# Kernel optimization log

Measured on AMD Instinct MI355X. Metric: run time of the kernel, lower is better.

The kernel has to match this reference:

```python
import jax, jax.numpy as jnp
import numpy as np

N_NODES = 50000
N_EDGES = 800000
NFEAT = 256
NHID = 512
BN_EPS = 1e-5


def setup_inputs() -> dict:
    key = jax.random.key(0)
    ks = jax.random.split(key, 6)
    x = jax.random.normal(ks[0], (N_NODES, NFEAT), dtype=jnp.float32)
    edge_index = jax.random.randint(ks[1], (2, N_EDGES), 0, N_NODES, dtype=jnp.int64)
    # Xavier-uniform linear weights, zero biases (matches weights_init)
    lim1 = np.sqrt(6.0 / (NFEAT + NHID))
    W1 = jax.random.uniform(ks[2], (NFEAT, NHID), minval=-lim1, maxval=lim1, dtype=jnp.float32)
    b1 = jnp.zeros((NHID,), dtype=jnp.float32)
    lim2 = np.sqrt(6.0 / (NHID + NHID))
    W2 = jax.random.uniform(ks[3], (NHID, NHID), minval=-lim2, maxval=lim2, dtype=jnp.float32)
    b2 = jnp.zeros((NHID,), dtype=jnp.float32)
    gamma = jnp.ones((NHID,), dtype=jnp.float32)
    beta = jnp.zeros((NHID,), dtype=jnp.float32)
    return {"x": x, "edge_index": edge_index, "W1": W1, "b1": b1,
            "gamma": gamma, "beta": beta, "W2": W2, "b2": b2}


def reference(x, edge_index, W1, b1, gamma, beta, W2, b2):
    # GINConv (eps=0): h_i = MLP(x_i + sum_{j->i} x_j)
    src = edge_index[0]
    dst = edge_index[1]
    agg = jax.ops.segment_sum(x[src], dst, num_segments=x.shape[0])  # [N, nfeat]
    h = x + agg
    # MLP: Linear -> ReLU -> BatchNorm1d (training-mode batch stats) -> Linear
    h = jax.nn.relu(h @ W1 + b1)  # [N, nhid]
    mean = jnp.mean(h, axis=0)
    var = jnp.var(h, axis=0)  # biased, as PyTorch uses for normalization
    h = (h - mean) * jax.lax.rsqrt(var + BN_EPS) * gamma + beta
    return h @ W2 + b2
```

## Files before the change

### kernel.cpp

```cpp
#include <hip/hip_runtime.h>

#define NNODES 50000
#define NF 256
#define NH 512
#define MPAD 50048
#define NRB 391
#define BN_EPS 1e-5f
#define NSCAN 196

typedef unsigned short u16;
typedef __attribute__((ext_vector_type(8))) short bf16x8;
typedef __attribute__((ext_vector_type(4))) float f32x4;

__device__ __forceinline__ float bf2f(u16 u) {
  union { unsigned int i; float f; } v; v.i = ((unsigned int)u) << 16; return v.f;
}
__device__ __forceinline__ u16 f2bf(float f) {
  union { float ff; unsigned int i; } v; v.ff = f;
  unsigned int r = v.i + 0x7FFFu + ((v.i >> 16) & 1u);
  return (u16)(r >> 16);
}

__device__ __forceinline__ void async16(const void* g, void* l) {
  __builtin_amdgcn_global_load_lds(
      (const __attribute__((address_space(1))) unsigned int*)g,
      (__attribute__((address_space(3))) unsigned int*)l, 16, 0, 0);
}

__global__ void detect_idx(const int* __restrict__ ei, int* __restrict__ flag) {
  int v = ei[2 * threadIdx.x + 1];
  unsigned long long b = __ballot(v == 0);
  if (threadIdx.x == 0) *flag = (b == ~0ull) ? 1 : 0;
}

__global__ __launch_bounds__(256) void prep_kernel(const float* __restrict__ x,
                                                   u16* __restrict__ xbf,
                                                   const float* __restrict__ W1,
                                                   u16* __restrict__ W1t,
                                                   const int* __restrict__ ei,
                                                   const int* __restrict__ flag,
                                                   int* __restrict__ deg, int E) {
  const int b = blockIdx.x;
  if (b < 2048) {
    const size_t n8 = (size_t)NNODES * NF / 8;
    size_t stride = (size_t)2048 * 256;
    for (size_t i = b * (size_t)256 + threadIdx.x; i < n8; i += stride) {
      float4 a = ((const float4*)x)[2 * i];
      float4 c = ((const float4*)x)[2 * i + 1];
      ushort4 lo, hi;
      lo.x = f2bf(a.x); lo.y = f2bf(a.y); lo.z = f2bf(a.z); lo.w = f2bf(a.w);
      hi.x = f2bf(c.x); hi.y = f2bf(c.y); hi.z = f2bf(c.z); hi.w = f2bf(c.w);
      ((ushort4*)xbf)[2 * i] = lo;
      ((ushort4*)xbf)[2 * i + 1] = hi;
    }
  } else if (b < 2560) {
    int idx = (b - 2048) * 256 + threadIdx.x;
    int n = idx >> 8;
    int k = idx & 255;
    W1t[(size_t)n * NF + k] = f2bf(W1[(size_t)k * NH + n]);
  } else {
    const int is64 = *flag;
    const int gtid = (b - 2560) * 256 + threadIdx.x;
    const int stride = 1024 * 256;
    if (is64) {
      const int4* d4 = (const int4*)(ei + 2 * (size_t)E);
      int np = E >> 1;
      for (int p = gtid; p < np; p += stride) {
        int4 d = d4[p];
        if ((unsigned)d.x < NNODES) atomicAdd(&deg[d.x], 1);
        if ((unsigned)d.z < NNODES) atomicAdd(&deg[d.z], 1);
      }
      for (int e = (np << 1) + gtid; e < E; e += stride) {
        int d = ei[2 * (size_t)E + 2 * e];
        if ((unsigned)d < NNODES) atomicAdd(&deg[d], 1);
      }
    } else {
      const int4* d4 = (const int4*)(ei + E);
      int np = E >> 2;
      for (int p = gtid; p < np; p += stride) {
        int4 d = d4[p];
        if ((unsigned)d.x < NNODES) atomicAdd(&deg[d.x], 1);
        if ((unsigned)d.y < NNODES) atomicAdd(&deg[d.y], 1);
        if ((unsigned)d.z < NNODES) atomicAdd(&deg[d.z], 1);
        if ((unsigned)d.w < NNODES) atomicAdd(&deg[d.w], 1);
      }
      for (int e = (np << 2) + gtid; e < E; e += stride) {
        int d = ei[(size_t)E + e];
        if ((unsigned)d < NNODES) atomicAdd(&deg[d], 1);
      }
    }
  }
}

__global__ __launch_bounds__(256) void scan1_kernel(const int* __restrict__ deg,
                                                    int* __restrict__ rowptr,
                                                    int* __restrict__ blocksums) {
  const int t = threadIdx.x;
  int i = blockIdx.x * 256 + t;
  int v = (i < NNODES) ? deg[i] : 0;
  __shared__ int sm[256];
  sm[t] = v;
  __syncthreads();
  for (int off = 1; off < 256; off <<= 1) {
    int u = (t >= off) ? sm[t - off] : 0;
    __syncthreads();
    sm[t] += u;
    __syncthreads();
  }
  if (i < NNODES) rowptr[i] = sm[t] - v;
  if (t == 255) blocksums[blockIdx.x] = sm[255];
}

__global__ __launch_bounds__(256) void scan2_kernel(int* __restrict__ blocksums,
                                                    int* __restrict__ rowptr) {
  const int t = threadIdx.x;
  int v = (t < NSCAN) ? blocksums[t] : 0;
  __shared__ int sm[256];
  sm[t] = v;
  __syncthreads();
  for (int off = 1; off < 256; off <<= 1) {
    int u = (t >= off) ? sm[t - off] : 0;
    __syncthreads();
    sm[t] += u;
    __syncthreads();
  }
  if (t < NSCAN) blocksums[t] = sm[t] - v;
  if (t == 255) rowptr[NNODES] = sm[255];
}

__global__ __launch_bounds__(256) void scan3_kernel(const int* __restrict__ blocksums,
                                                    int* __restrict__ rowptr) {
  int i = blockIdx.x * 256 + threadIdx.x;
  if (i < NNODES) rowptr[i] += blocksums[blockIdx.x];
}

__global__ __launch_bounds__(256) void fill_kernel(const int* __restrict__ ei,
                                                   const int* __restrict__ flag,
                                                   const int* __restrict__ rowptr,
                                                   int* __restrict__ cursor,
                                                   int* __restrict__ srcs, int E) {
  const int is64 = *flag;
  const int gtid = blockIdx.x * 256 + threadIdx.x;
  const int stride = gridDim.x * 256;
  if (is64) {
    const int4* s4 = (const int4*)ei;
    const int4* d4 = (const int4*)(ei + 2 * (size_t)E);
    int np = E >> 1;
    for (int p = gtid; p < np; p += stride) {
      int4 sv = s4[p], dv = d4[p];
      if ((unsigned)sv.x < NNODES && (unsigned)dv.x < NNODES) {
        int pos = rowptr[dv.x] + atomicAdd(&cursor[dv.x], 1);
        if ((unsigned)pos < (unsigned)E) srcs[pos] = sv.x;
      }
      if ((unsigned)sv.z < NNODES && (unsigned)dv.z < NNODES) {
        int pos = rowptr[dv.z] + atomicAdd(&cursor[dv.z], 1);
        if ((unsigned)pos < (unsigned)E) srcs[pos] = sv.z;
      }
    }
    for (int e = (np << 1) + gtid; e < E; e += stride) {
      int src = ei[2 * e], dst = ei[2 * (size_t)E + 2 * e];
      if ((unsigned)src >= NNODES || (unsigned)dst >= NNODES) continue;
      int pos = rowptr[dst] + atomicAdd(&cursor[dst], 1);
      if ((unsigned)pos < (unsigned)E) srcs[pos] = src;
    }
  } else {
    const int4* s4 = (const int4*)ei;
    const int4* d4 = (const int4*)(ei + E);
    int np = E >> 2;
    for (int p = gtid; p < np; p += stride) {
      int4 sv = s4[p], dv = d4[p];
      int ss[4] = {sv.x, sv.y, sv.z, sv.w};
      int dd[4] = {dv.x, dv.y, dv.z, dv.w};
#pragma unroll
      for (int j = 0; j < 4; ++j) {
        if ((unsigned)ss[j] < NNODES && (unsigned)dd[j] < NNODES) {
          int pos = rowptr[dd[j]] + atomicAdd(&cursor[dd[j]], 1);
          if ((unsigned)pos < (unsigned)E) srcs[pos] = ss[j];
        }
      }
    }
    for (int e = (np << 2) + gtid; e < E; e += stride) {
      int src = ei[e], dst = ei[(size_t)E + e];
      if ((unsigned)src >= NNODES || (unsigned)dst >= NNODES) continue;
      int pos = rowptr[dst] + atomicAdd(&cursor[dst], 1);
      if ((unsigned)pos < (unsigned)E) srcs[pos] = src;
    }
  }
}

__global__ __launch_bounds__(256) void gather_kernel(const u16* __restrict__ xbf,
                                                     const int* __restrict__ srcs,
                                                     const int* __restrict__ rowptr,
                                                     u16* __restrict__ hpad) {
  const int hl = threadIdx.x & 31;
  const int node = blockIdx.x * 8 + (threadIdx.x >> 5);
  if (node >= MPAD) return;
  bf16x8* outp = (bf16x8*)(hpad + (size_t)node * NF + hl * 8);
  if (node >= NNODES) {
    bf16x8 z = {0, 0, 0, 0, 0, 0, 0, 0};
    *outp = z;
    return;
  }
  bf16x8 sv = *(const bf16x8*)(xbf + (size_t)node * NF + hl * 8);
  float acc[8];
#pragma unroll
  for (int j = 0; j < 8; ++j) acc[j] = bf2f((u16)sv[j]);
  int e = rowptr[node];
  const int e1 = rowptr[node + 1];
  for (; e + 3 < e1; e += 4) {
    int s0 = srcs[e], s1 = srcs[e + 1], s2 = srcs[e + 2], s3 = srcs[e + 3];
    bf16x8 v0 = *(const bf16x8*)(xbf + (size_t)s0 * NF + hl * 8);
    bf16x8 v1 = *(const bf16x8*)(xbf + (size_t)s1 * NF + hl * 8);
    bf16x8 v2 = *(const bf16x8*)(xbf + (size_t)s2 * NF + hl * 8);
    bf16x8 v3 = *(const bf16x8*)(xbf + (size_t)s3 * NF + hl * 8);
#pragma unroll
    for (int j = 0; j < 8; ++j)
      acc[j] += bf2f((u16)v0[j]) + bf2f((u16)v1[j]) + bf2f((u16)v2[j]) + bf2f((u16)v3[j]);
  }
  for (; e < e1; ++e) {
    int s0 = srcs[e];
    bf16x8 v0 = *(const bf16x8*)(xbf + (size_t)s0 * NF + hl * 8);
#pragma unroll
    for (int j = 0; j < 8; ++j) acc[j] += bf2f((u16)v0[j]);
  }
  bf16x8 o;
#pragma unroll
  for (int j = 0; j < 8; ++j) o[j] = (short)f2bf(acc[j]);
  *outp = o;
}

template <int K, bool RELU, bool OUTF32, bool STATS>
__global__ __launch_bounds__(256) void gemm_bt(const u16* __restrict__ Ab,
                                               const u16* __restrict__ Bt,
                                               const float* __restrict__ bias,
                                               void* __restrict__ Cp, int Mstore,
                                               float* __restrict__ parts) {
  __shared__ __align__(16) u16 As[2][128 * 64];
  __shared__ __align__(16) u16 Bs[2][128 * 64];
  __shared__ float sred[256];
  const int tid = threadIdx.x;
  const int lane = tid & 63;
  const int wid = tid >> 6;
  const int wr = wid >> 1, wc = wid & 1;

  const int nwg = gridDim.x;
  const int q = nwg >> 3, r = nwg & 7;
  const int xcd = blockIdx.x & 7, idx = blockIdx.x >> 3;
  const int work = (xcd < r ? xcd * (q + 1) : r * (q + 1) + (xcd - r) * q) + idx;
  const int brow = (work >> 2) * 128;
  const int bcol = (work & 3) * 128;

  f32x4 acc[4][4] = {};

  const int lrow = lane >> 3;
  const int lkc = ((lane & 7) ^ (lrow & 7)) * 8;
  const int nt = K / 64;

#pragma unroll
  for (int i = 0; i < 4; ++i) {
    int c = i * 4 + wid;
    int row = c * 8 + lrow;
    async16(Ab + (size_t)(brow + row) * K + lkc, &As[0][c * 512]);
    async16(Bt + (size_t)(bcol + row) * K + lkc, &Bs[0][c * 512]);
  }
  if (STATS) {
    if (tid < 64) ((float4*)sred)[tid] = (float4){0.f, 0.f, 0.f, 0.f};
  }
  __syncthreads();

  int cur = 0;
  for (int t = 0; t < nt; ++t) {
    if (t + 1 < nt) {
      const int k0 = (t + 1) * 64;
#pragma unroll
      for (int i = 0; i < 4; ++i) {
        int c = i * 4 + wid;
        int row = c * 8 + lrow;
        async16(Ab + (size_t)(brow + row) * K + k0 + lkc, &As[cur ^ 1][c * 512]);
        async16(Bt + (size_t)(bcol + row) * K + k0 + lkc, &Bs[cur ^ 1][c * 512]);
      }
    }
#pragma unroll
    for (int ks = 0; ks < 2; ++ks) {
      bf16x8 af[4], bfr[4];
      const int rchunk = ((ks << 2) + (lane >> 4)) ^ (lane & 7);
#pragma unroll
      for (int m = 0; m < 4; ++m)
        af[m] = *(const bf16x8*)&As[cur][(wr * 64 + m * 16 + (lane & 15)) * 64 + rchunk * 8];
#pragma unroll
      for (int n = 0; n < 4; ++n)
        bfr[n] = *(const bf16x8*)&Bs[cur][(wc * 64 + n * 16 + (lane & 15)) * 64 + rchunk * 8];
#pragma unroll
      for (int n = 0; n < 4; ++n)
#pragma unroll
        for (int m = 0; m < 4; ++m)
          acc[n][m] = __builtin_amdgcn_mfma_f32_16x16x32_bf16(bfr[n], af[m], acc[n][m], 0, 0, 0);
    }
    __syncthreads();
    cur ^= 1;
  }

  const int row_base = brow + wr * 64 + (lane & 15);
  const int col_base = bcol + wc * 64 + ((lane >> 4) << 2);
#pragma unroll
  for (int n = 0; n < 4; ++n) {
    int col = col_base + n * 16;
    float4 bv4 = *(const float4*)&bias[col];
    float s0 = 0.f, s1 = 0.f, s2 = 0.f, s3 = 0.f;
    float q0 = 0.f, q1 = 0.f, q2 = 0.f, q3 = 0.f;
#pragma unroll
    for (int m = 0; m < 4; ++m) {
      int row = row_base + m * 16;
      f32x4 a = acc[n][m];
      float v0 = a[0] + bv4.x, v1 = a[1] + bv4.y, v2 = a[2] + bv4.z, v3 = a[3] + bv4.w;
      if (RELU) {
        v0 = fmaxf(v0, 0.f); v1 = fmaxf(v1, 0.f);
        v2 = fmaxf(v2, 0.f); v3 = fmaxf(v3, 0.f);
      }
      if (row < Mstore) {
        if (OUTF32) {
          float4 o = {v0, v1, v2, v3};
          *(float4*)&((float*)Cp)[(size_t)row * NH + col] = o;
        } else {
          ushort4 o = {f2bf(v0), f2bf(v1), f2bf(v2), f2bf(v3)};
          *(ushort4*)&((u16*)Cp)[(size_t)row * NH + col] = o;
        }
      }
      if (STATS && row < NNODES) {
        s0 += v0; s1 += v1; s2 += v2; s3 += v3;
        q0 += v0 * v0; q1 += v1 * v1; q2 += v2 * v2; q3 += v3 * v3;
      }
    }
    if (STATS) {
#pragma unroll
      for (int msk = 1; msk < 16; msk <<= 1) {
        s0 += __shfl_xor(s0, msk); s1 += __shfl_xor(s1, msk);
        s2 += __shfl_xor(s2, msk); s3 += __shfl_xor(s3, msk);
        q0 += __shfl_xor(q0, msk); q1 += __shfl_xor(q1, msk);
        q2 += __shfl_xor(q2, msk); q3 += __shfl_xor(q3, msk);
      }
      if ((lane & 15) == 0) {
        int lc = wc * 64 + n * 16 + ((lane >> 4) << 2);
        atomicAdd(&sred[lc + 0], s0); atomicAdd(&sred[lc + 1], s1);
        atomicAdd(&sred[lc + 2], s2); atomicAdd(&sred[lc + 3], s3);
        atomicAdd(&sred[128 + lc + 0], q0); atomicAdd(&sred[128 + lc + 1], q1);
        atomicAdd(&sred[128 + lc + 2], q2); atomicAdd(&sred[128 + lc + 3], q3);
      }
    }
  }
  if (STATS) {
    __syncthreads();
    if (tid < 128) {
      parts[(size_t)work * 256 + tid] = sred[tid];
      parts[(size_t)work * 256 + 128 + tid] = sred[128 + tid];
    }
  }
}

__global__ __launch_bounds__(256) void stats2_kernel(const float* __restrict__ parts,
                                                     float* __restrict__ ssum) {
  int c = blockIdx.x * 256 + threadIdx.x;
  int c0 = c & 511, issq = c >> 9;
  float acc = 0.f;
  for (int rb = 0; rb < NRB; ++rb)
    acc += parts[(size_t)((rb << 2) + (c0 >> 7)) * 256 + (c0 & 127) + (issq ? 128 : 0)];
  ssum[c] = acc;
}

__global__ void bn_finalize(const float* __restrict__ ssum, const float* __restrict__ ssq,
                            const float* __restrict__ gamma, const float* __restrict__ beta,
                            float* __restrict__ a_arr, float* __restrict__ c_arr,
                            int* __restrict__ err) {
  int c = threadIdx.x;
  float mean = ssum[c] * (1.f / NNODES);
  float var = ssq[c] * (1.f / NNODES) - mean * mean;
  if (!(mean == mean) || !(var == var) ||
      fabsf(mean) > 1e20f || var > 1e20f || var < -1e-2f)
    err[0] = 2;
  unsigned long long z = __ballot(ssq[c] == 0.0f);
  if (threadIdx.x == 0 && z == ~0ull) err[1] = 3;
  if (var < 0.f) var = 0.f;
  float a = gamma[c] * rsqrtf(var + BN_EPS);
  a_arr[c] = a;
  c_arr[c] = beta[c] - mean * a;
}

__global__ __launch_bounds__(256) void fold_w2(const float* __restrict__ W2,
                                               const float* __restrict__ b2,
                                               const float* __restrict__ a_arr,
                                               const float* __restrict__ c_arr,
                                               u16* __restrict__ W2pt,
                                               float* __restrict__ bias2p) {
  int n = blockIdx.x;
  int t = threadIdx.x;
  float accv = 0.f;
  for (int k = t; k < NH; k += 256) {
    float w = W2[(size_t)k * NH + n];
    W2pt[(size_t)n * NH + k] = f2bf(a_arr[k] * w);
    accv += c_arr[k] * w;
  }
  __shared__ float red[256];
  red[t] = accv;
  __syncthreads();
  for (int s = 128; s > 0; s >>= 1) {
    if (t < s) red[t] += red[t + s];
    __syncthreads();
  }
  if (t == 0) bias2p[n] = b2[n] + red[0];
}

__global__ __launch_bounds__(256) void write_sentinel(float* __restrict__ out, int n, float val) {
  int stride = gridDim.x * blockDim.x;
  for (int i = blockIdx.x * blockDim.x + threadIdx.x; i < n; i += stride) out[i] = val;
}

__global__ __launch_bounds__(256) void apply_err(const int* __restrict__ err,
                                                 float* __restrict__ out, int n) {
  float val = 0.f;
  if (err[1] == 3) val = -300000.f;
  if (err[0] == 2) val = -500000.f;
  if (val == 0.f) return;
  int stride = gridDim.x * blockDim.x;
  for (int i = blockIdx.x * blockDim.x + threadIdx.x; i < n; i += stride) out[i] = val;
}

extern "C" void kernel_launch(void* const* d_in, const int* in_sizes, int n_in,
                              void* d_out, int out_size, void* d_ws, size_t ws_size,
                              hipStream_t stream) {
  const float* x     = (const float*)d_in[0];
  const int*   ei    = (const int*)d_in[1];
  const float* W1    = (const float*)d_in[2];
  const float* b1    = (const float*)d_in[3];
  const float* gamma = (const float*)d_in[4];
  const float* beta  = (const float*)d_in[5];
  const float* W2    = (const float*)d_in[6];
  const float* b2    = (const float*)d_in[7];
  float* out = (float*)d_out;
  const int E = in_sizes[1] / 2;

  char* ws = (char*)d_ws;
  size_t off = 0;
  auto alloc = [&](size_t bytes) {
    char* p = ws + off;
    off += (bytes + 255) & ~(size_t)255;
    return p;
  };
  u16*   xbf    = (u16*)alloc((size_t)NNODES * NF * 2);
  u16*   hpad   = (u16*)alloc((size_t)MPAD * NF * 2);
  u16*   h1     = (u16*)alloc((size_t)MPAD * NH * 2);
  u16*   W1t    = (u16*)alloc((size_t)NH * NF * 2);
  u16*   W2pt   = (u16*)alloc((size_t)NH * NH * 2);
  int*   srcs   = (int*)alloc((size_t)E * 4);
  int*   rowptr = (int*)alloc((size_t)(NNODES + 1) * 4);
  int*   deg    = (int*)alloc((size_t)2 * NNODES * 4);
  int*   cursor = deg + NNODES;
  int*   bsums  = (int*)alloc(256 * 4);
  float* parts  = (float*)alloc((size_t)NRB * 4 * 256 * 4);
  float* ssum   = (float*)alloc(NH * 4);
  float* ssq    = (float*)alloc(NH * 4);
  int*   err    = (int*)alloc(8);
  float* a_arr  = (float*)alloc(NH * 4);
  float* c_arr  = (float*)alloc(NH * 4);
  float* bias2p = (float*)alloc(NH * 4);
  int*   flag   = (int*)alloc(4);

  if (off > ws_size) {
    write_sentinel<<<2048, 256, 0, stream>>>(out, out_size,
        1.0e7f + 1048576.0f * (float)(ws_size >> 20));
    return;
  }

  hipMemsetAsync(deg, 0, (size_t)2 * NNODES * 4, stream);
  hipMemsetAsync(err, 0, 8, stream);

  detect_idx<<<1, 64, 0, stream>>>(ei, flag);
  prep_kernel<<<3584, 256, 0, stream>>>(x, xbf, W1, W1t, ei, flag, deg, E);
  scan1_kernel<<<NSCAN, 256, 0, stream>>>(deg, rowptr, bsums);
  scan2_kernel<<<1, 256, 0, stream>>>(bsums, rowptr);
  scan3_kernel<<<NSCAN, 256, 0, stream>>>(bsums, rowptr);
  fill_kernel<<<1024, 256, 0, stream>>>(ei, flag, rowptr, cursor, srcs, E);
  gather_kernel<<<MPAD / 8, 256, 0, stream>>>(xbf, srcs, rowptr, hpad);

  const int nwg = NRB * 4;
  gemm_bt<NF, true, false, true><<<nwg, 256, 0, stream>>>(hpad, W1t, b1, h1, MPAD, parts);

  stats2_kernel<<<4, 256, 0, stream>>>(parts, ssum);
  bn_finalize<<<1, NH, 0, stream>>>(ssum, ssq, gamma, beta, a_arr, c_arr, err);
  fold_w2<<<NH, 256, 0, stream>>>(W2, b2, a_arr, c_arr, W2pt, bias2p);

  gemm_bt<NH, false, true, false><<<nwg, 256, 0, stream>>>(h1, W2pt, bias2p, out, NNODES, nullptr);

  apply_err<<<2048, 256, 0, stream>>>(err, out, out_size);
}
```

Baseline: 284.1 us.

## Cut kernel launches by fusing scan, fill, conversion and BN stats stages

Index-format detection moves into the histogram and fill kernels, so its separate launch goes away. The three-pass scan becomes two passes, with the second pass also writing a cursor array holding absolute offsets, which removes the rowptr load per edge in the fill. The CSR fill is combined with the x-to-bf16 conversion and the W1 transpose in one launch, so the bandwidth-bound conversion can overlap the atomic-heavy fill. The stats reduction is merged with BN finalize, and the zero-variance error sentinel is dropped. The cost is that each scan_b block recomputes the block-sums scan, and the prep work now waits on the histogram and scan.

```diff
diff --git a/kernel.cpp b/kernel.cpp
--- a/kernel.cpp
+++ b/kernel.cpp
@@ -27,74 +27,49 @@
       (__attribute__((address_space(3))) unsigned int*)l, 16, 0, 0);
 }
 
-__global__ void detect_idx(const int* __restrict__ ei, int* __restrict__ flag) {
-  int v = ei[2 * threadIdx.x + 1];
-  unsigned long long b = __ballot(v == 0);
-  if (threadIdx.x == 0) *flag = (b == ~0ull) ? 1 : 0;
-}
-
-__global__ __launch_bounds__(256) void prep_kernel(const float* __restrict__ x,
-                                                   u16* __restrict__ xbf,
-                                                   const float* __restrict__ W1,
-                                                   u16* __restrict__ W1t,
-                                                   const int* __restrict__ ei,
-                                                   const int* __restrict__ flag,
+__global__ __launch_bounds__(256) void hist_kernel(const int* __restrict__ ei,
                                                    int* __restrict__ deg, int E) {
-  const int b = blockIdx.x;
-  if (b < 2048) {
-    const size_t n8 = (size_t)NNODES * NF / 8;
-    size_t stride = (size_t)2048 * 256;
-    for (size_t i = b * (size_t)256 + threadIdx.x; i < n8; i += stride) {
-      float4 a = ((const float4*)x)[2 * i];
-      float4 c = ((const float4*)x)[2 * i + 1];
-      ushort4 lo, hi;
-      lo.x = f2bf(a.x); lo.y = f2bf(a.y); lo.z = f2bf(a.z); lo.w = f2bf(a.w);
-      hi.x = f2bf(c.x); hi.y = f2bf(c.y); hi.z = f2bf(c.z); hi.w = f2bf(c.w);
-      ((ushort4*)xbf)[2 * i] = lo;
-      ((ushort4*)xbf)[2 * i + 1] = hi;
-    }
-  } else if (b < 2560) {
-    int idx = (b - 2048) * 256 + threadIdx.x;
-    int n = idx >> 8;
-    int k = idx & 255;
-    W1t[(size_t)n * NF + k] = f2bf(W1[(size_t)k * NH + n]);
+  __shared__ int sf;
+  if (threadIdx.x < 64) {
+    unsigned long long b = __ballot(ei[2 * threadIdx.x + 1] == 0);
+    if (threadIdx.x == 0) sf = (b == ~0ull) ? 1 : 0;
+  }
+  __syncthreads();
+  const int is64 = sf;
+  const int gtid = blockIdx.x * 256 + threadIdx.x;
+  const int stride = gridDim.x * 256;
+  if (is64) {
+    const int4* d4 = (const int4*)(ei + 2 * (size_t)E);
+    int np = E >> 1;
+    for (int p = gtid; p < np; p += stride) {
+      int4 d = d4[p];
+      if ((unsigned)d.x < NNODES) atomicAdd(&deg[d.x], 1);
+      if ((unsigned)d.z < NNODES) atomicAdd(&deg[d.z], 1);
+    }
+    for (int e = (np << 1) + gtid; e < E; e += stride) {
+      int d = ei[2 * (size_t)E + 2 * e];
+      if ((unsigned)d < NNODES) atomicAdd(&deg[d], 1);
+    }
   } else {
-    const int is64 = *flag;
-    const int gtid = (b - 2560) * 256 + threadIdx.x;
-    const int stride = 1024 * 256;
-    if (is64) {
-      const int4* d4 = (const int4*)(ei + 2 * (size_t)E);
-      int np = E >> 1;
-      for (int p = gtid; p < np; p += stride) {
-        int4 d = d4[p];
-        if ((unsigned)d.x < NNODES) atomicAdd(&deg[d.x], 1);
-        if ((unsigned)d.z < NNODES) atomicAdd(&deg[d.z], 1);
-      }
-      for (int e = (np << 1) + gtid; e < E; e += stride) {
-        int d = ei[2 * (size_t)E + 2 * e];
-        if ((unsigned)d < NNODES) atomicAdd(&deg[d], 1);
-      }
-    } else {
-      const int4* d4 = (const int4*)(ei + E);
-      int np = E >> 2;
-      for (int p = gtid; p < np; p += stride) {
-        int4 d = d4[p];
-        if ((unsigned)d.x < NNODES) atomicAdd(&deg[d.x], 1);
-        if ((unsigned)d.y < NNODES) atomicAdd(&deg[d.y], 1);
-        if ((unsigned)d.z < NNODES) atomicAdd(&deg[d.z], 1);
-        if ((unsigned)d.w < NNODES) atomicAdd(&deg[d.w], 1);
-      }
-      for (int e = (np << 2) + gtid; e < E; e += stride) {
-        int d = ei[(size_t)E + e];
-        if ((unsigned)d < NNODES) atomicAdd(&deg[d], 1);
-      }
-    }
-  }
-}
-
-__global__ __launch_bounds__(256) void scan1_kernel(const int* __restrict__ deg,
-                                                    int* __restrict__ rowptr,
-                                                    int* __restrict__ blocksums) {
+    const int4* d4 = (const int4*)(ei + E);
+    int np = E >> 2;
+    for (int p = gtid; p < np; p += stride) {
+      int4 d = d4[p];
+      if ((unsigned)d.x < NNODES) atomicAdd(&deg[d.x], 1);
+      if ((unsigned)d.y < NNODES) atomicAdd(&deg[d.y], 1);
+      if ((unsigned)d.z < NNODES) atomicAdd(&deg[d.z], 1);
+      if ((unsigned)d.w < NNODES) atomicAdd(&deg[d.w], 1);
+    }
+    for (int e = (np << 2) + gtid; e < E; e += stride) {
+      int d = ei[(size_t)E + e];
+      if ((unsigned)d < NNODES) atomicAdd(&deg[d], 1);
+    }
+  }
+}
+
+__global__ __launch_bounds__(256) void scan_a(const int* __restrict__ deg,
+                                              int* __restrict__ rowptr,
+                                              int* __restrict__ blocksums) {
   const int t = threadIdx.x;
   int i = blockIdx.x * 256 + t;
   int v = (i < NNODES) ? deg[i] : 0;
@@ -111,12 +86,12 @@
   if (t == 255) blocksums[blockIdx.x] = sm[255];
 }
 
-__global__ __launch_bounds__(256) void scan2_kernel(int* __restrict__ blocksums,
-                                                    int* __restrict__ rowptr) {
+__global__ __launch_bounds__(256) void scan_b(const int* __restrict__ blocksums,
+                                              int* __restrict__ rowptr,
+                                              int* __restrict__ cw) {
   const int t = threadIdx.x;
-  int v = (t < NSCAN) ? blocksums[t] : 0;
   __shared__ int sm[256];
-  sm[t] = v;
+  sm[t] = (t < NSCAN) ? blocksums[t] : 0;
   __syncthreads();
   for (int off = 1; off < 256; off <<= 1) {
     int u = (t >= off) ? sm[t - off] : 0;
@@ -124,67 +99,95 @@
     sm[t] += u;
     __syncthreads();
   }
-  if (t < NSCAN) blocksums[t] = sm[t] - v;
-  if (t == 255) rowptr[NNODES] = sm[255];
-}
-
-__global__ __launch_bounds__(256) void scan3_kernel(const int* __restrict__ blocksums,
-                                                    int* __restrict__ rowptr) {
-  int i = blockIdx.x * 256 + threadIdx.x;
-  if (i < NNODES) rowptr[i] += blocksums[blockIdx.x];
-}
-
-__global__ __launch_bounds__(256) void fill_kernel(const int* __restrict__ ei,
-                                                   const int* __restrict__ flag,
-                                                   const int* __restrict__ rowptr,
-                                                   int* __restrict__ cursor,
-                                                   int* __restrict__ srcs, int E) {
-  const int is64 = *flag;
-  const int gtid = blockIdx.x * 256 + threadIdx.x;
-  const int stride = gridDim.x * 256;
-  if (is64) {
-    const int4* s4 = (const int4*)ei;
-    const int4* d4 = (const int4*)(ei + 2 * (size_t)E);
-    int np = E >> 1;
-    for (int p = gtid; p < np; p += stride) {
-      int4 sv = s4[p], dv = d4[p];
-      if ((unsigned)sv.x < NNODES && (unsigned)dv.x < NNODES) {
-        int pos = rowptr[dv.x] + atomicAdd(&cursor[dv.x], 1);
-        if ((unsigned)pos < (unsigned)E) srcs[pos] = sv.x;
-      }
-      if ((unsigned)sv.z < NNODES && (unsigned)dv.z < NNODES) {
-        int pos = rowptr[dv.z] + atomicAdd(&cursor[dv.z], 1);
-        if ((unsigned)pos < (unsigned)E) srcs[pos] = sv.z;
-      }
-    }
-    for (int e = (np << 1) + gtid; e < E; e += stride) {
-      int src = ei[2 * e], dst = ei[2 * (size_t)E + 2 * e];
-      if ((unsigned)src >= NNODES || (unsigned)dst >= NNODES) continue;
-      int pos = rowptr[dst] + atomicAdd(&cursor[dst], 1);
-      if ((unsigned)pos < (unsigned)E) srcs[pos] = src;
+  const int boff = (blockIdx.x == 0) ? 0 : sm[blockIdx.x - 1];
+  int i = blockIdx.x * 256 + t;
+  if (i < NNODES) {
+    int rv = rowptr[i] + boff;
+    rowptr[i] = rv;
+    cw[i] = rv;
+  }
+  if (blockIdx.x == 0 && t == 0) rowptr[NNODES] = sm[NSCAN - 1];
+}
+
+__global__ __launch_bounds__(256) void fused_kernel(const int* __restrict__ ei, int E,
+                                                    int* __restrict__ cw,
+                                                    int* __restrict__ srcs,
+                                                    const float* __restrict__ x,
+                                                    u16* __restrict__ xbf,
+                                                    const float* __restrict__ W1,
+                                                    u16* __restrict__ W1t) {
+  const int b = blockIdx.x;
+  if (b < 1024) {
+    __shared__ int sf;
+    if (threadIdx.x < 64) {
+      unsigned long long bb = __ballot(ei[2 * threadIdx.x + 1] == 0);
+      if (threadIdx.x == 0) sf = (bb == ~0ull) ? 1 : 0;
+    }
+    __syncthreads();
+    const int is64 = sf;
+    const int gtid = b * 256 + threadIdx.x;
+    const int stride = 1024 * 256;
+    if (is64) {
+      const int4* s4 = (const int4*)ei;
+      const int4* d4 = (const int4*)(ei + 2 * (size_t)E);
+      int np = E >> 1;
+      for (int p = gtid; p < np; p += stride) {
+        int4 sv = s4[p], dv = d4[p];
+        if ((unsigned)sv.x < NNODES && (unsigned)dv.x < NNODES) {
+          int pos = atomicAdd(&cw[dv.x], 1);
+          if ((unsigned)pos < (unsigned)E) srcs[pos] = sv.x;
+        }
+        if ((unsigned)sv.z < NNODES && (unsigned)dv.z < NNODES) {
+          int pos = atomicAdd(&cw[dv.z], 1);
+          if ((unsigned)pos < (unsigned)E) srcs[pos] = sv.z;
+        }
+      }
+      for (int e = (np << 1) + gtid; e < E; e += stride) {
+        int src = ei[2 * e], dst = ei[2 * (size_t)E + 2 * e];
+        if ((unsigned)src >= NNODES || (unsigned)dst >= NNODES) continue;
+        int pos = atomicAdd(&cw[dst], 1);
+        if ((unsigned)pos < (unsigned)E) srcs[pos] = src;
+      }
+    } else {
+      const int4* s4 = (const int4*)ei;
+      const int4* d4 = (const int4*)(ei + E);
+      int np = E >> 2;
+      for (int p = gtid; p < np; p += stride) {
+        int4 sv = s4[p], dv = d4[p];
+        int ss[4] = {sv.x, sv.y, sv.z, sv.w};
+        int dd[4] = {dv.x, dv.y, dv.z, dv.w};
+#pragma unroll
+        for (int j = 0; j < 4; ++j) {
+          if ((unsigned)ss[j] < NNODES && (unsigned)dd[j] < NNODES) {
+            int pos = atomicAdd(&cw[dd[j]], 1);
+            if ((unsigned)pos < (unsigned)E) srcs[pos] = ss[j];
+          }
+        }
+      }
+      for (int e = (np << 2) + gtid; e < E; e += stride) {
+        int src = ei[e], dst = ei[(size_t)E + e];
+        if ((unsigned)src >= NNODES || (unsigned)dst >= NNODES) continue;
+        int pos = atomicAdd(&cw[dst], 1);
+        if ((unsigned)pos < (unsigned)E) srcs[pos] = src;
+      }
+    }
+  } else if (b < 3072) {
+    const size_t n8 = (size_t)NNODES * NF / 8;
+    size_t stride = (size_t)2048 * 256;
+    for (size_t i = (b - 1024) * (size_t)256 + threadIdx.x; i < n8; i += stride) {
+      float4 a = ((const float4*)x)[2 * i];
+      float4 c = ((const float4*)x)[2 * i + 1];
+      ushort4 lo, hi;
+      lo.x = f2bf(a.x); lo.y = f2bf(a.y); lo.z = f2bf(a.z); lo.w = f2bf(a.w);
+      hi.x = f2bf(c.x); hi.y = f2bf(c.y); hi.z = f2bf(c.z); hi.w = f2bf(c.w);
+      ((ushort4*)xbf)[2 * i] = lo;
+      ((ushort4*)xbf)[2 * i + 1] = hi;
     }
   } else {
-    const int4* s4 = (const int4*)ei;
-    const int4* d4 = (const int4*)(ei + E);
-    int np = E >> 2;
-    for (int p = gtid; p < np; p += stride) {
-      int4 sv = s4[p], dv = d4[p];
-      int ss[4] = {sv.x, sv.y, sv.z, sv.w};
-      int dd[4] = {dv.x, dv.y, dv.z, dv.w};
-#pragma unroll
-      for (int j = 0; j < 4; ++j) {
-        if ((unsigned)ss[j] < NNODES && (unsigned)dd[j] < NNODES) {
-          int pos = rowptr[dd[j]] + atomicAdd(&cursor[dd[j]], 1);
-          if ((unsigned)pos < (unsigned)E) srcs[pos] = ss[j];
-        }
-      }
-    }
-    for (int e = (np << 2) + gtid; e < E; e += stride) {
-      int src = ei[e], dst = ei[(size_t)E + e];
-      if ((unsigned)src >= NNODES || (unsigned)dst >= NNODES) continue;
-      int pos = rowptr[dst] + atomicAdd(&cursor[dst], 1);
-      if ((unsigned)pos < (unsigned)E) srcs[pos] = src;
-    }
+    int idx = (b - 3072) * 256 + threadIdx.x;
+    int n = idx >> 8;
+    int k = idx & 255;
+    W1t[(size_t)n * NF + k] = f2bf(W1[(size_t)k * NH + n]);
   }
 }
 
@@ -357,28 +360,25 @@
   }
 }
 
-__global__ __launch_bounds__(256) void stats2_kernel(const float* __restrict__ parts,
-                                                     float* __restrict__ ssum) {
+__global__ __launch_bounds__(256) void stats_bn(const float* __restrict__ parts,
+                                                const float* __restrict__ gamma,
+                                                const float* __restrict__ beta,
+                                                float* __restrict__ a_arr,
+                                                float* __restrict__ c_arr,
+                                                int* __restrict__ err) {
   int c = blockIdx.x * 256 + threadIdx.x;
-  int c0 = c & 511, issq = c >> 9;
-  float acc = 0.f;
-  for (int rb = 0; rb < NRB; ++rb)
-    acc += parts[(size_t)((rb << 2) + (c0 >> 7)) * 256 + (c0 & 127) + (issq ? 128 : 0)];
-  ssum[c] = acc;
-}
-
-__global__ void bn_finalize(const float* __restrict__ ssum, const float* __restrict__ ssq,
-                            const float* __restrict__ gamma, const float* __restrict__ beta,
-                            float* __restrict__ a_arr, float* __restrict__ c_arr,
-                            int* __restrict__ err) {
-  int c = threadIdx.x;
-  float mean = ssum[c] * (1.f / NNODES);
-  float var = ssq[c] * (1.f / NNODES) - mean * mean;
+  int grp = (c >> 7) & 3, cl = c & 127;
+  float s = 0.f, qq = 0.f;
+  for (int rb = 0; rb < NRB; ++rb) {
+    const float* p = parts + (size_t)((rb << 2) + grp) * 256 + cl;
+    s += p[0];
+    qq += p[128];
+  }
+  float mean = s * (1.f / NNODES);
+  float var = qq * (1.f / NNODES) - mean * mean;
   if (!(mean == mean) || !(var == var) ||
       fabsf(mean) > 1e20f || var > 1e20f || var < -1e-2f)
     err[0] = 2;
-  unsigned long long z = __ballot(ssq[c] == 0.0f);
-  if (threadIdx.x == 0 && z == ~0ull) err[1] = 3;
   if (var < 0.f) var = 0.f;
   float a = gamma[c] * rsqrtf(var + BN_EPS);
   a_arr[c] = a;
@@ -416,12 +416,9 @@
 
 __global__ __launch_bounds__(256) void apply_err(const int* __restrict__ err,
                                                  float* __restrict__ out, int n) {
-  float val = 0.f;
-  if (err[1] == 3) val = -300000.f;
-  if (err[0] == 2) val = -500000.f;
-  if (val == 0.f) return;
+  if (err[0] == 0) return;
   int stride = gridDim.x * blockDim.x;
-  for (int i = blockIdx.x * blockDim.x + threadIdx.x; i < n; i += stride) out[i] = val;
+  for (int i = blockIdx.x * blockDim.x + threadIdx.x; i < n; i += stride) out[i] = -500000.f;
 }
 
 extern "C" void kernel_launch(void* const* d_in, const int* in_sizes, int n_in,
@@ -452,17 +449,14 @@
   u16*   W2pt   = (u16*)alloc((size_t)NH * NH * 2);
   int*   srcs   = (int*)alloc((size_t)E * 4);
   int*   rowptr = (int*)alloc((size_t)(NNODES + 1) * 4);
-  int*   deg    = (int*)alloc((size_t)2 * NNODES * 4);
-  int*   cursor = deg + NNODES;
+  int*   cw     = (int*)alloc((size_t)NNODES * 4);
+  int*   deg    = (int*)alloc((size_t)NNODES * 4);
   int*   bsums  = (int*)alloc(256 * 4);
   float* parts  = (float*)alloc((size_t)NRB * 4 * 256 * 4);
-  float* ssum   = (float*)alloc(NH * 4);
-  float* ssq    = (float*)alloc(NH * 4);
   int*   err    = (int*)alloc(8);
   float* a_arr  = (float*)alloc(NH * 4);
   float* c_arr  = (float*)alloc(NH * 4);
   float* bias2p = (float*)alloc(NH * 4);
-  int*   flag   = (int*)alloc(4);
 
   if (off > ws_size) {
     write_sentinel<<<2048, 256, 0, stream>>>(out, out_size,
@@ -470,22 +464,19 @@
     return;
   }
 
-  hipMemsetAsync(deg, 0, (size_t)2 * NNODES * 4, stream);
+  hipMemsetAsync(deg, 0, (size_t)NNODES * 4, stream);
   hipMemsetAsync(err, 0, 8, stream);
 
-  detect_idx<<<1, 64, 0, stream>>>(ei, flag);
-  prep_kernel<<<3584, 256, 0, stream>>>(x, xbf, W1, W1t, ei, flag, deg, E);
-  scan1_kernel<<<NSCAN, 256, 0, stream>>>(deg, rowptr, bsums);
-  scan2_kernel<<<1, 256, 0, stream>>>(bsums, rowptr);
-  scan3_kernel<<<NSCAN, 256, 0, stream>>>(bsums, rowptr);
-  fill_kernel<<<1024, 256, 0, stream>>>(ei, flag, rowptr, cursor, srcs, E);
+  hist_kernel<<<1024, 256, 0, stream>>>(ei, deg, E);
+  scan_a<<<NSCAN, 256, 0, stream>>>(deg, rowptr, bsums);
+  scan_b<<<NSCAN, 256, 0, stream>>>(bsums, rowptr, cw);
+  fused_kernel<<<3584, 256, 0, stream>>>(ei, E, cw, srcs, x, xbf, W1, W1t);
   gather_kernel<<<MPAD / 8, 256, 0, stream>>>(xbf, srcs, rowptr, hpad);
 
   const int nwg = NRB * 4;
   gemm_bt<NF, true, false, true><<<nwg, 256, 0, stream>>>(hpad, W1t, b1, h1, MPAD, parts);
 
-  stats2_kernel<<<4, 256, 0, stream>>>(parts, ssum);
-  bn_finalize<<<1, NH, 0, stream>>>(ssum, ssq, gamma, beta, a_arr, c_arr, err);
+  stats_bn<<<2, 256, 0, stream>>>(parts, gamma, beta, a_arr, c_arr, err);
   fold_w2<<<NH, 256, 0, stream>>>(W2, b2, a_arr, c_arr, W2pt, bias2p);
 
   gemm_bt<NH, false, true, false><<<nwg, 256, 0, stream>>>(h1, W2pt, bias2p, out, NNODES, nullptr);
```

After: 315.9 us. 1.11x slower.
